# Performance work log

Measured on AMD Instinct MI355X. Metric: run time of the kernel, lower is better.

The kernel has to match this reference:

```python
import jax, jax.numpy as jnp
import numpy as np
import math

DIM = 1536; NH = 12; HD = 128
F, H, W = 6, 30, 30
S = F * H * W
B = 1
K_LEN = 9900  # hardcoded k_lens in the source forward
EPS_NORM = 1e-6


def _rope_tables(max_len=1024, d=HD):
    # Wan rope_params: three tables of widths d-4*(d//6), 2*(d//6), 2*(d//6)
    # -> cos/sin tables of half-widths 22, 21, 21 (concat = d//2 = 64)
    def ang(dd):
        inv = 1.0 / (10000.0 ** (np.arange(0, dd, 2, dtype=np.float64) / dd))
        return np.outer(np.arange(max_len, dtype=np.float64), inv)
    a = np.concatenate([ang(d - 4 * (d // 6)), ang(2 * (d // 6)), ang(2 * (d // 6))], axis=1)
    return np.cos(a).astype(np.float32), np.sin(a).astype(np.float32)


def setup_inputs() -> dict:
    key = jax.random.key(0)
    ks = jax.random.split(key, 5)
    s = 1.0 / math.sqrt(DIM)
    cos, sin = _rope_tables()
    return {
        "x": jax.random.normal(ks[0], (B, S, DIM), jnp.float32),
        "q_w": jax.random.normal(ks[1], (DIM, DIM), jnp.float32) * s,
        "q_b": jnp.zeros((DIM,), jnp.float32),
        "k_w": jax.random.normal(ks[2], (DIM, DIM), jnp.float32) * s,
        "k_b": jnp.zeros((DIM,), jnp.float32),
        "v_w": jax.random.normal(ks[3], (DIM, DIM), jnp.float32) * s,
        "v_b": jnp.zeros((DIM,), jnp.float32),
        "o_w": jax.random.normal(ks[4], (DIM, DIM), jnp.float32) * s,
        "o_b": jnp.zeros((DIM,), jnp.float32),
        "norm_q_w": jnp.ones((DIM,), jnp.float32),
        "norm_k_w": jnp.ones((DIM,), jnp.float32),
        "freqs_cos": jnp.asarray(cos),
        "freqs_sin": jnp.asarray(sin),
        "grid_f": F, "grid_h": H, "grid_w": W,
    }


def rms_norm(x, w):
    # RMSNorm over full model dim, computed in fp32 (as in source)
    xf = x.astype(jnp.float32)
    xn = xf * jax.lax.rsqrt(jnp.mean(xf * xf, axis=-1, keepdims=True) + EPS_NORM)
    return xn.astype(x.dtype) * w


def rope_apply(x, cos, sin, f, h, w):
    # x: [B,S,N,D]; rotate consecutive pairs with 3D-factorized (f,h,w) freqs
    Bb, Ss, Nn, Dd = x.shape
    c = Dd // 2
    sp = [c - 2 * (c // 3), c // 3, c // 3]  # 22, 21, 21

    def grid(tab):
        tf = tab[:, :sp[0]]
        th = tab[:, sp[0]:sp[0] + sp[1]]
        tw = tab[:, sp[0] + sp[1]:]
        g = jnp.concatenate([
            jnp.broadcast_to(tf[:f, None, None, :], (f, h, w, sp[0])),
            jnp.broadcast_to(th[None, :h, None, :], (f, h, w, sp[1])),
            jnp.broadcast_to(tw[None, None, :w, :], (f, h, w, sp[2])),
        ], axis=-1)
        return g.reshape(f * h * w, 1, c)  # [S,1,c] (broadcast over heads)

    gc, gs = grid(cos), grid(sin)
    xp = x.astype(jnp.float32).reshape(Bb, Ss, Nn, c, 2)
    xr, xi = xp[..., 0], xp[..., 1]
    orr = xr * gc - xi * gs
    oii = xr * gs + xi * gc
    return jnp.stack([orr, oii], axis=-1).reshape(Bb, Ss, Nn, Dd).astype(x.dtype)


def attention(q, k, v, k_len):
    # full attention (window_size=(-1,-1)) with keys masked beyond k_len
    scale = 1.0 / math.sqrt(q.shape[-1])
    att = jnp.einsum('bqnd,bknd->bnqk', q, k) * scale
    valid = jnp.arange(k.shape[1]) < k_len
    att = jnp.where(valid[None, None, None, :], att, jnp.finfo(att.dtype).min)
    p = jax.nn.softmax(att, axis=-1)
    return jnp.einsum('bnqk,bknd->bqnd', p, v)


def reference(x, q_w, q_b, k_w, k_b, v_w, v_b, o_w, o_b, norm_q_w, norm_k_w, freqs_cos, freqs_sin, grid_f, grid_h, grid_w):
    Bb, Ss, _ = x.shape
    q = rms_norm(x @ q_w.T + q_b, norm_q_w).reshape(Bb, Ss, NH, HD)
    k = rms_norm(x @ k_w.T + k_b, norm_k_w).reshape(Bb, Ss, NH, HD)
    v = (x @ v_w.T + v_b).reshape(Bb, Ss, NH, HD)
    q = rope_apply(q, freqs_cos, freqs_sin, grid_f, grid_h, grid_w)
    k = rope_apply(k, freqs_cos, freqs_sin, grid_f, grid_h, grid_w)
    o = attention(q, k, v, K_LEN).reshape(Bb, Ss, NH * HD)
    return o @ o_w.T + o_b
```

## Files before the change

kernel.cpp:

```cpp
#include <hip/hip_runtime.h>

#define DIM 1536
#define NH 12
#define HD 128
#define S_LEN 5400
#define SPAD 5504
#define MPAD 5504
#define NQKV 4608
#define EPS_NORM 1e-6f

typedef __bf16 bf16_t;
typedef __bf16 bf16x8 __attribute__((ext_vector_type(8)));
typedef __bf16 bf16x4 __attribute__((ext_vector_type(4)));
typedef __bf16 bf16x2 __attribute__((ext_vector_type(2)));
typedef float  f32x4  __attribute__((ext_vector_type(4)));
typedef float  f32x16 __attribute__((ext_vector_type(16)));
typedef int    i32x2  __attribute__((ext_vector_type(2)));

#define GLOAD_LDS16(gp, lp) __builtin_amdgcn_global_load_lds( \
    (__attribute__((address_space(1))) void*)(void*)(gp),     \
    (__attribute__((address_space(3))) void*)(lp), 16, 0, 0)

__device__ __forceinline__ unsigned int pkbf(float a, float b) {
  union { bf16x2 h; unsigned int u; } c;
  c.h[0] = (__bf16)a; c.h[1] = (__bf16)b;
  return c.u;
}

__device__ __forceinline__ float xhalf_max(float x) {
  i32x2 r = __builtin_amdgcn_permlane32_swap(__float_as_int(x), __float_as_int(x),
                                             false, false);
  return fmaxf(__int_as_float(r.x), __int_as_float(r.y));
}
__device__ __forceinline__ float xhalf_sum(float x) {
  i32x2 r = __builtin_amdgcn_permlane32_swap(__float_as_int(x), __float_as_int(x),
                                             false, false);
  return __int_as_float(r.x) + __int_as_float(r.y);
}


__global__ __launch_bounds__(256) void cvt_x_kernel(const float* __restrict__ x,
                                                    bf16_t* __restrict__ xb) {
  size_t base = ((size_t)blockIdx.x * 256 + threadIdx.x) * 4;
  if (base >= (size_t)MPAD * DIM) return;
  size_t row = base / DIM;
  float4 v = make_float4(0.f, 0.f, 0.f, 0.f);
  if (row < S_LEN) v = *(const float4*)&x[base];
  bf16x4 o; o[0] = (__bf16)v.x; o[1] = (__bf16)v.y; o[2] = (__bf16)v.z; o[3] = (__bf16)v.w;
  *(bf16x4*)&xb[base] = o;
}

__global__ __launch_bounds__(256) void cvt_wqkv_kernel(const float* __restrict__ qw,
                                                       const float* __restrict__ kw,
                                                       const float* __restrict__ vw,
                                                       bf16_t* __restrict__ wb) {
  size_t base = ((size_t)blockIdx.x * 256 + threadIdx.x) * 4;
  if (base >= (size_t)NQKV * DIM) return;
  int row = (int)(base / DIM);
  int col = (int)(base - (size_t)row * DIM);
  const float* src; int rr = row;
  if (rr >= 3072)      { src = vw; rr -= 3072; }
  else if (rr >= 1536) { src = kw; rr -= 1536; }
  else                 { src = qw; }
  float4 v = *(const float4*)&src[(size_t)rr * DIM + col];
  bf16x4 o; o[0] = (__bf16)v.x; o[1] = (__bf16)v.y; o[2] = (__bf16)v.z; o[3] = (__bf16)v.w;
  *(bf16x4*)&wb[base] = o;
}

__global__ __launch_bounds__(256) void cvt_wo_kernel(const float* __restrict__ w,
                                                     bf16_t* __restrict__ wb) {
  size_t base = ((size_t)blockIdx.x * 256 + threadIdx.x) * 4;
  if (base >= (size_t)DIM * DIM) return;
  float4 v = *(const float4*)&w[base];
  bf16x4 o; o[0] = (__bf16)v.x; o[1] = (__bf16)v.y; o[2] = (__bf16)v.z; o[3] = (__bf16)v.w;
  *(bf16x4*)&wb[base] = o;
}


template<bool OUT_BF16>
__global__ __launch_bounds__(256) void gemm_bt_kernel(
    const bf16_t* __restrict__ A, const bf16_t* __restrict__ B, void* __restrict__ C,
    const float* __restrict__ bias0, const float* __restrict__ bias1,
    const float* __restrict__ bias2, int M, int N, int K, int Mvalid) {
  __shared__ bf16_t As[2][128 * 32];
  __shared__ bf16_t Bs[2][128 * 32];
  int tid = threadIdx.x;
  int lane = tid & 63, wave = tid >> 6, quad = lane >> 4, l16 = lane & 15;
  int m0 = blockIdx.y * 128, n0 = blockIdx.x * 128;
  int wm = (wave >> 1) * 64, wn = (wave & 1) * 64;
  const bf16_t* Ab = A + (size_t)m0 * K;
  const bf16_t* Bb = B + (size_t)n0 * K;
  f32x4 acc[4][4] = {};

  int eo0 = tid * 8;
  int row0 = eo0 >> 5, col0 = eo0 & 31;
  int eo1 = (256 + tid) * 8;
  int row1 = eo1 >> 5, col1 = eo1 & 31;

  GLOAD_LDS16(Ab + (size_t)row0 * K + col0, &As[0][eo0]);
  GLOAD_LDS16(Bb + (size_t)row0 * K + col0, &Bs[0][eo0]);
  GLOAD_LDS16(Ab + (size_t)row1 * K + col1, &As[0][eo1]);
  GLOAD_LDS16(Bb + (size_t)row1 * K + col1, &Bs[0][eo1]);
  asm volatile("s_waitcnt vmcnt(0)" ::: "memory");
  __builtin_amdgcn_s_barrier();
  __builtin_amdgcn_sched_barrier(0);

  int KT = K >> 5;
  for (int t = 0; t < KT; t++) {
    int cur = t & 1;
    if (t + 1 < KT) {
      int kn = (t + 1) << 5;
      GLOAD_LDS16(Ab + (size_t)row0 * K + kn + col0, &As[cur ^ 1][eo0]);
      GLOAD_LDS16(Bb + (size_t)row0 * K + kn + col0, &Bs[cur ^ 1][eo0]);
      GLOAD_LDS16(Ab + (size_t)row1 * K + kn + col1, &As[cur ^ 1][eo1]);
      GLOAD_LDS16(Bb + (size_t)row1 * K + kn + col1, &Bs[cur ^ 1][eo1]);
    }
    bf16x8 af[4], bfr[4];
#pragma unroll
    for (int i = 0; i < 4; i++)
      af[i] = *(const bf16x8*)&As[cur][(wm + i * 16 + l16) * 32 + quad * 8];
#pragma unroll
    for (int j = 0; j < 4; j++)
      bfr[j] = *(const bf16x8*)&Bs[cur][(wn + j * 16 + l16) * 32 + quad * 8];
#pragma unroll
    for (int i = 0; i < 4; i++)
#pragma unroll
      for (int j = 0; j < 4; j++)
        acc[i][j] = __builtin_amdgcn_mfma_f32_16x16x32_bf16(af[i], bfr[j], acc[i][j], 0, 0, 0);
    asm volatile("s_waitcnt vmcnt(0) lgkmcnt(0)" ::: "memory");
    __builtin_amdgcn_s_barrier();
    __builtin_amdgcn_sched_barrier(0);
  }
#pragma unroll
  for (int j = 0; j < 4; j++) {
    int n = n0 + wn + j * 16 + l16;
    float bias = (n < 1536) ? bias0[n] : (n < 3072) ? bias1[n - 1536] : bias2[n - 3072];
#pragma unroll
    for (int i = 0; i < 4; i++) {
#pragma unroll
      for (int r = 0; r < 4; r++) {
        int m = m0 + wm + i * 16 + quad * 4 + r;
        float v = acc[i][j][r] + bias;
        if (OUT_BF16) {
          ((bf16_t*)C)[(size_t)m * N + n] = (__bf16)v;
        } else {
          if (m < Mvalid) ((float*)C)[(size_t)m * N + n] = v;
        }
      }
    }
  }
}


__global__ __launch_bounds__(256) void rope_qk_kernel(
    const bf16_t* __restrict__ qkv, const float* __restrict__ nqw,
    const float* __restrict__ nkw, const float* __restrict__ fcos,
    const float* __restrict__ fsin, bf16_t* __restrict__ qout,
    bf16_t* __restrict__ kout) {
  int s = blockIdx.x;
  int tid = threadIdx.x;
  bool valid = s < S_LEN;
  int f = s / 900, hh = (s / 30) % 30, ww = s % 30;
  __shared__ float red[4];
  for (int which = 0; which < 2; which++) {
    const bf16_t* src = qkv + (size_t)s * NQKV + which * DIM;
    const float* nw = which ? nkw : nqw;
    bf16_t* dst = (which ? kout : qout) + (size_t)s * DIM;
    float osc = which ? 1.0f : 0.12751742686f;
    float v[6]; float ss = 0.f;
#pragma unroll
    for (int i = 0; i < 6; i++) {
      v[i] = valid ? (float)src[tid * 6 + i] : 0.f;
      ss += v[i] * v[i];
    }
#pragma unroll
    for (int off = 32; off >= 1; off >>= 1) ss += __shfl_down(ss, off);
    if ((tid & 63) == 0) red[tid >> 6] = ss;
    __syncthreads();
    float tot = red[0] + red[1] + red[2] + red[3];
    float rn = rsqrtf(tot * (1.f / DIM) + EPS_NORM);
    __syncthreads();
#pragma unroll
    for (int i = 0; i < 3; i++) {
      int e0 = tid * 6 + 2 * i;
      int p = e0 >> 1;
      int cc = p & 63;
      int pos = (cc < 22) ? f : (cc < 43) ? hh : ww;
      float c = fcos[pos * 64 + cc], sn = fsin[pos * 64 + cc];
      float xr = v[2 * i] * rn * nw[e0];
      float xi = v[2 * i + 1] * rn * nw[e0 + 1];
      dst[e0]     = (__bf16)((xr * c - xi * sn) * osc);
      dst[e0 + 1] = (__bf16)((xr * sn + xi * c) * osc);
    }
  }
}


__global__ __launch_bounds__(256) void v_transpose_kernel(const bf16_t* __restrict__ qkv,
                                                          bf16_t* __restrict__ vt) {
  __shared__ bf16_t tile[64][136];
  int h = blockIdx.y, s0 = blockIdx.x * 64, tid = threadIdx.x;
#pragma unroll
  for (int it = 0; it < 4; it++) {
    int eo = (it * 256 + tid) * 8;
    int row = eo >> 7, col = eo & 127;
    int s = s0 + row;
    bf16x8 val = {};
    if (s < S_LEN) val = *(const bf16x8*)&qkv[(size_t)s * NQKV + 3072 + h * HD + col];
    *(bf16x8*)&tile[row][col] = val;
  }
  __syncthreads();
  int d = tid & 127, j0 = (tid >> 7) * 32;
  bf16x8 outv[4];
#pragma unroll
  for (int b = 0; b < 4; b++)
#pragma unroll
    for (int j = 0; j < 8; j++) outv[b][j] = tile[j0 + b * 8 + j][d];
  size_t base = ((size_t)h * HD + d) * SPAD + s0 + j0;
#pragma unroll
  for (int b = 0; b < 4; b++) *(bf16x8*)&vt[base + b * 8] = outv[b];
}


__global__ __launch_bounds__(256, 2) void flash_attn_kernel(
    const bf16_t* __restrict__ q, const bf16_t* __restrict__ k,
    const bf16_t* __restrict__ vt, bf16_t* __restrict__ o) {
  __shared__ __align__(16) char lds_raw[65536];
  bf16_t* Ks = (bf16_t*)lds_raw;
  bf16_t* Vs = (bf16_t*)(lds_raw + 32768);
  int nwg = gridDim.x;
  int bid = blockIdx.x;
  int xcd = bid & 7, idx = bid >> 3;
  int q8 = nwg >> 3, rr = nwg & 7;
  int work = (xcd < rr ? xcd * (q8 + 1) : rr * (q8 + 1) + (xcd - rr) * q8) + idx;
  int head = work / 43;
  int s0 = (work - head * 43) * 128;

  int tid = threadIdx.x, w = tid >> 6, lane = tid & 63;
  int l31 = lane & 31, hh = lane >> 5;

  bf16x8 bq[8];
  {
    const bf16_t* qp = &q[(size_t)(s0 + w * 32 + l31) * DIM + head * HD + hh * 8];
#pragma unroll
    for (int kc = 0; kc < 8; kc++) bq[kc] = *(const bf16x8*)(qp + kc * 16);
  }

  float m_i = -1e30f, l_i = 0.f;
  f32x16 oacc[4] = {};

  const int NT = SPAD / 128;

  for (int t = 0; t < NT; t++) {
    int kt = t * 128;

#pragma unroll
    for (int it = 0; it < 8; it++) {
      int slot = it * 256 + tid;
      int row = slot >> 4, pc = slot & 15;
      int c = pc ^ (row & 15);
      GLOAD_LDS16(k + (size_t)(kt + row) * DIM + head * HD + c * 8, &Ks[slot * 8]);
    }
#pragma unroll
    for (int h2 = 0; h2 < 2; h2++)
#pragma unroll
      for (int it = 0; it < 4; it++) {
        int slot = it * 256 + tid;
        int row = slot >> 4, pc = slot & 15;
        int cp = pc ^ (row & 15);
        int d = 2 * row + (cp >> 3);
        GLOAD_LDS16(vt + ((size_t)head * HD + d) * SPAD + kt + h2 * 64 + (cp & 7) * 8,
                    &Vs[h2 * 8192 + slot * 8]);
      }
    asm volatile("s_waitcnt vmcnt(0)" ::: "memory");
    __builtin_amdgcn_s_barrier();
    __builtin_amdgcn_sched_barrier(0);

    f32x16 sacc[4] = {};
    __builtin_amdgcn_s_setprio(1);
#pragma unroll
    for (int ns = 0; ns < 4; ns++) {
      int row = ns * 32 + l31;
#pragma unroll
      for (int kc = 0; kc < 8; kc++) {
        int pc = (kc * 2 + hh) ^ (row & 15);
        bf16x8 ak = *(const bf16x8*)&Ks[row * 128 + pc * 8];
        sacc[ns] = __builtin_amdgcn_mfma_f32_32x32x16_bf16(ak, bq[kc], sacc[ns], 0, 0, 0);
      }
    }
    __builtin_amdgcn_s_setprio(0);

    if (kt + 128 > S_LEN) {
#pragma unroll
      for (int ns = 0; ns < 4; ns++)
#pragma unroll
        for (int r = 0; r < 16; r++) {
          int kvg = kt + ns * 32 + (r & 3) + 8 * (r >> 2) + 4 * hh;
          if (kvg >= S_LEN) sacc[ns][r] = -1e30f;
        }
    }

    float mx;
    {
      float tm[8];
#pragma unroll
      for (int i = 0; i < 8; i++) {
        float a = fmaxf(fmaxf(sacc[0][i], sacc[0][i + 8]),
                        fmaxf(sacc[1][i], sacc[1][i + 8]));
        float b = fmaxf(fmaxf(sacc[2][i], sacc[2][i + 8]),
                        fmaxf(sacc[3][i], sacc[3][i + 8]));
        tm[i] = fmaxf(a, b);
      }
#pragma unroll
      for (int i = 0; i < 4; i++) tm[i] = fmaxf(tm[i], tm[i + 4]);
      mx = fmaxf(fmaxf(tm[0], tm[2]), fmaxf(tm[1], tm[3]));
    }
    mx = xhalf_max(mx);
    if (!__all(mx - m_i <= 11.5f)) {
      float mn = fmaxf(m_i, mx);
      float al = __builtin_amdgcn_exp2f(m_i - mn);
      l_i *= al;
#pragma unroll
      for (int dt = 0; dt < 4; dt++)
#pragma unroll
        for (int r = 0; r < 16; r++) oacc[dt][r] *= al;
      m_i = mn;
    }
#pragma unroll
    for (int ns = 0; ns < 4; ns++)
#pragma unroll
      for (int r = 0; r < 16; r++)
        sacc[ns][r] = __builtin_amdgcn_exp2f(sacc[ns][r] - m_i);
    float rs;
    {
      float ts[8];
#pragma unroll
      for (int i = 0; i < 8; i++)
        ts[i] = ((sacc[0][i] + sacc[0][i + 8]) + (sacc[1][i] + sacc[1][i + 8])) +
                ((sacc[2][i] + sacc[2][i + 8]) + (sacc[3][i] + sacc[3][i + 8]));
#pragma unroll
      for (int i = 0; i < 4; i++) ts[i] += ts[i + 4];
      rs = (ts[0] + ts[2]) + (ts[1] + ts[3]);
    }
    l_i += xhalf_sum(rs);

    __builtin_amdgcn_s_setprio(1);
#pragma unroll
    for (int kvc = 0; kvc < 8; kvc++) {
      int ns = kvc >> 1, rb = (kvc & 1) * 8;
      int w0 = (int)pkbf(sacc[ns][rb + 0], sacc[ns][rb + 1]);
      int w1 = (int)pkbf(sacc[ns][rb + 2], sacc[ns][rb + 3]);
      int w2 = (int)pkbf(sacc[ns][rb + 4], sacc[ns][rb + 5]);
      int w3 = (int)pkbf(sacc[ns][rb + 6], sacc[ns][rb + 7]);
      i32x2 r02 = __builtin_amdgcn_permlane32_swap(w0, w2, false, false);
      i32x2 r13 = __builtin_amdgcn_permlane32_swap(w1, w3, false, false);
      union { unsigned int u[4]; bf16x8 v8; } bpu;
      bpu.u[0] = (unsigned int)r02.x; bpu.u[1] = (unsigned int)r13.x;
      bpu.u[2] = (unsigned int)r02.y; bpu.u[3] = (unsigned int)r13.y;
      bf16x8 bp = bpu.v8;
      int h2 = kvc >> 2, kvl = kvc & 3;
      const bf16_t* Vh = Vs + h2 * 8192;
#pragma unroll
      for (int dt = 0; dt < 4; dt++) {
        int d = dt * 32 + l31;
        int r = d >> 1;
        int cp = ((d & 1) << 3) | (kvl * 2 + hh);
        int pc = cp ^ (r & 15);
        bf16x8 av = *(const bf16x8*)&Vh[r * 128 + pc * 8];
        oacc[dt] = __builtin_amdgcn_mfma_f32_32x32x16_bf16(av, bp, oacc[dt], 0, 0, 0);
      }
    }
    __builtin_amdgcn_s_setprio(0);

    asm volatile("s_waitcnt lgkmcnt(0)" ::: "memory");
    __builtin_amdgcn_s_barrier();
    __builtin_amdgcn_sched_barrier(0);
  }

  bf16_t* scr = Ks + w * (32 * 64);
  float inv = 1.f / l_i;
  int qr = lane >> 1, seg = lane & 1;
  int srow = s0 + w * 32 + qr;
#pragma unroll
  for (int half = 0; half < 2; half++) {
#pragma unroll
    for (int dl = 0; dl < 2; dl++) {
      int dt = half * 2 + dl;
#pragma unroll
      for (int tt = 0; tt < 4; tt++) {
        bf16x4 v;
#pragma unroll
        for (int r4 = 0; r4 < 4; r4++) v[r4] = (__bf16)(oacc[dt][tt * 4 + r4] * inv);
        int c8 = dl * 8 + 2 * tt + hh;
        int pc8 = c8 ^ (l31 & 15);
        *(bf16x4*)&scr[l31 * 64 + pc8 * 4] = v;
      }
    }
#pragma unroll
    for (int i = 0; i < 4; i++) {
      int c8 = seg * 8 + 2 * i;
      bf16x4 lo = *(const bf16x4*)&scr[qr * 64 + ((c8) ^ (qr & 15)) * 4];
      bf16x4 hi = *(const bf16x4*)&scr[qr * 64 + ((c8 + 1) ^ (qr & 15)) * 4];
      bf16x8 val;
#pragma unroll
      for (int j = 0; j < 4; j++) { val[j] = lo[j]; val[j + 4] = hi[j]; }
      if (srow < S_LEN)
        *(bf16x8*)&o[(size_t)srow * DIM + head * HD + half * 64 + seg * 32 + i * 8] = val;
    }
  }
}


extern "C" void kernel_launch(void* const* d_in, const int* in_sizes, int n_in,
                              void* d_out, int out_size, void* d_ws, size_t ws_size,
                              hipStream_t stream) {
  const float* x    = (const float*)d_in[0];
  const float* q_w  = (const float*)d_in[1];
  const float* q_b  = (const float*)d_in[2];
  const float* k_w  = (const float*)d_in[3];
  const float* k_b  = (const float*)d_in[4];
  const float* v_w  = (const float*)d_in[5];
  const float* v_b  = (const float*)d_in[6];
  const float* o_w  = (const float*)d_in[7];
  const float* o_b  = (const float*)d_in[8];
  const float* nqw  = (const float*)d_in[9];
  const float* nkw  = (const float*)d_in[10];
  const float* fcos = (const float*)d_in[11];
  const float* fsin = (const float*)d_in[12];

  char* ws = (char*)d_ws;
  bf16_t* xb   = (bf16_t*)(ws + 0);
  bf16_t* wqkv = (bf16_t*)(ws + 16908288);
  bf16_t* wob  = (bf16_t*)(ws + 31064064);
  bf16_t* qkv  = (bf16_t*)(ws + 35782656);
  bf16_t* qb   = (bf16_t*)(ws + 86507520);
  bf16_t* kb   = (bf16_t*)(ws + 103415808);
  bf16_t* vtb  = (bf16_t*)(ws + 0);
  bf16_t* aob  = (bf16_t*)(ws + 35782656);

  cvt_x_kernel<<<(MPAD * DIM / 4 + 255) / 256, 256, 0, stream>>>(x, xb);
  cvt_wqkv_kernel<<<(NQKV * DIM / 4 + 255) / 256, 256, 0, stream>>>(q_w, k_w, v_w, wqkv);
  cvt_wo_kernel<<<(DIM * DIM / 4 + 255) / 256, 256, 0, stream>>>(o_w, wob);

  gemm_bt_kernel<true><<<dim3(NQKV / 128, MPAD / 128), 256, 0, stream>>>(
      xb, wqkv, qkv, q_b, k_b, v_b, MPAD, NQKV, DIM, MPAD);

  rope_qk_kernel<<<MPAD, 256, 0, stream>>>(qkv, nqw, nkw, fcos, fsin, qb, kb);
  v_transpose_kernel<<<dim3(SPAD / 64, NH), 256, 0, stream>>>(qkv, vtb);

  flash_attn_kernel<<<dim3((MPAD / 128) * NH), 256, 0, stream>>>(qb, kb, vtb, aob);

  gemm_bt_kernel<false><<<dim3(DIM / 128, MPAD / 128), 256, 0, stream>>>(
      aob, wob, d_out, o_b, o_b, o_b, MPAD, DIM, DIM, S_LEN);
}
```

Before: 657.1 us.

## Load K/V tiles directly from global into registers, dropping LDS staging

Replaces cooperative LDS staging of K and V tiles with per-wave direct global loads into registers. It also halves the KV tile to 64 rows per iteration. This removes the workgroup barriers and LDS traffic each iteration. In exchange, every wave refetches the same K/V data, which multiplies global/L2 traffic, and load latency is no longer overlapped through shared staging.

```diff
diff --git a/kernel.cpp b/kernel.cpp
--- a/kernel.cpp
+++ b/kernel.cpp
@@ -225,9 +225,7 @@
 __global__ __launch_bounds__(256, 2) void flash_attn_kernel(
     const bf16_t* __restrict__ q, const bf16_t* __restrict__ k,
     const bf16_t* __restrict__ vt, bf16_t* __restrict__ o) {
-  __shared__ __align__(16) char lds_raw[65536];
-  bf16_t* Ks = (bf16_t*)lds_raw;
-  bf16_t* Vs = (bf16_t*)(lds_raw + 32768);
+  __shared__ __align__(16) bf16_t scr_all[4][32 * 64];
   int nwg = gridDim.x;
   int bid = blockIdx.x;
   int xcd = bid & 7, idx = bid >> 3;
@@ -246,53 +244,43 @@
     for (int kc = 0; kc < 8; kc++) bq[kc] = *(const bf16x8*)(qp + kc * 16);
   }
 
+  const bf16_t* kp = k + (size_t)l31 * DIM + head * HD + hh * 8;
+  const bf16_t* vp = vt + ((size_t)head * HD + l31) * SPAD + hh * 8;
+
   float m_i = -1e30f, l_i = 0.f;
   f32x16 oacc[4] = {};
 
-  const int NT = SPAD / 128;
+  const int NT = 85;
 
   for (int t = 0; t < NT; t++) {
-    int kt = t * 128;
-
-#pragma unroll
-    for (int it = 0; it < 8; it++) {
-      int slot = it * 256 + tid;
-      int row = slot >> 4, pc = slot & 15;
-      int c = pc ^ (row & 15);
-      GLOAD_LDS16(k + (size_t)(kt + row) * DIM + head * HD + c * 8, &Ks[slot * 8]);
-    }
-#pragma unroll
-    for (int h2 = 0; h2 < 2; h2++)
-#pragma unroll
-      for (int it = 0; it < 4; it++) {
-        int slot = it * 256 + tid;
-        int row = slot >> 4, pc = slot & 15;
-        int cp = pc ^ (row & 15);
-        int d = 2 * row + (cp >> 3);
-        GLOAD_LDS16(vt + ((size_t)head * HD + d) * SPAD + kt + h2 * 64 + (cp & 7) * 8,
-                    &Vs[h2 * 8192 + slot * 8]);
-      }
-    asm volatile("s_waitcnt vmcnt(0)" ::: "memory");
-    __builtin_amdgcn_s_barrier();
-    __builtin_amdgcn_sched_barrier(0);
-
-    f32x16 sacc[4] = {};
+    int kt = t * 64;
+
+    bf16x8 ak[16];
+#pragma unroll
+    for (int ns = 0; ns < 2; ns++)
+#pragma unroll
+      for (int kc = 0; kc < 8; kc++)
+        ak[ns * 8 + kc] = *(const bf16x8*)(kp + (size_t)(kt + ns * 32) * DIM + kc * 16);
+
+    f32x16 sacc[2] = {};
     __builtin_amdgcn_s_setprio(1);
 #pragma unroll
-    for (int ns = 0; ns < 4; ns++) {
-      int row = ns * 32 + l31;
-#pragma unroll
-      for (int kc = 0; kc < 8; kc++) {
-        int pc = (kc * 2 + hh) ^ (row & 15);
-        bf16x8 ak = *(const bf16x8*)&Ks[row * 128 + pc * 8];
-        sacc[ns] = __builtin_amdgcn_mfma_f32_32x32x16_bf16(ak, bq[kc], sacc[ns], 0, 0, 0);
-      }
-    }
+    for (int ns = 0; ns < 2; ns++)
+#pragma unroll
+      for (int kc = 0; kc < 8; kc++)
+        sacc[ns] = __builtin_amdgcn_mfma_f32_32x32x16_bf16(ak[ns * 8 + kc], bq[kc], sacc[ns], 0, 0, 0);
     __builtin_amdgcn_s_setprio(0);
 
-    if (kt + 128 > S_LEN) {
-#pragma unroll
-      for (int ns = 0; ns < 4; ns++)
+    bf16x8 av[16];
+#pragma unroll
+    for (int kvc = 0; kvc < 4; kvc++)
+#pragma unroll
+      for (int dt = 0; dt < 4; dt++)
+        av[kvc * 4 + dt] = *(const bf16x8*)(vp + (size_t)(dt * 32) * SPAD + kt + kvc * 16);
+
+    if (kt + 64 > S_LEN) {
+#pragma unroll
+      for (int ns = 0; ns < 2; ns++)
 #pragma unroll
         for (int r = 0; r < 16; r++) {
           int kvg = kt + ns * 32 + (r & 3) + 8 * (r >> 2) + 4 * hh;
@@ -304,13 +292,9 @@
     {
       float tm[8];
 #pragma unroll
-      for (int i = 0; i < 8; i++) {
-        float a = fmaxf(fmaxf(sacc[0][i], sacc[0][i + 8]),
-                        fmaxf(sacc[1][i], sacc[1][i + 8]));
-        float b = fmaxf(fmaxf(sacc[2][i], sacc[2][i + 8]),
-                        fmaxf(sacc[3][i], sacc[3][i + 8]));
-        tm[i] = fmaxf(a, b);
-      }
+      for (int i = 0; i < 8; i++)
+        tm[i] = fmaxf(fmaxf(sacc[0][i], sacc[0][i + 8]),
+                      fmaxf(sacc[1][i], sacc[1][i + 8]));
 #pragma unroll
       for (int i = 0; i < 4; i++) tm[i] = fmaxf(tm[i], tm[i + 4]);
       mx = fmaxf(fmaxf(tm[0], tm[2]), fmaxf(tm[1], tm[3]));
@@ -327,7 +311,7 @@
       m_i = mn;
     }
 #pragma unroll
-    for (int ns = 0; ns < 4; ns++)
+    for (int ns = 0; ns < 2; ns++)
 #pragma unroll
       for (int r = 0; r < 16; r++)
         sacc[ns][r] = __builtin_amdgcn_exp2f(sacc[ns][r] - m_i);
@@ -336,8 +320,7 @@
       float ts[8];
 #pragma unroll
       for (int i = 0; i < 8; i++)
-        ts[i] = ((sacc[0][i] + sacc[0][i + 8]) + (sacc[1][i] + sacc[1][i + 8])) +
-                ((sacc[2][i] + sacc[2][i + 8]) + (sacc[3][i] + sacc[3][i + 8]));
+        ts[i] = (sacc[0][i] + sacc[0][i + 8]) + (sacc[1][i] + sacc[1][i + 8]);
 #pragma unroll
       for (int i = 0; i < 4; i++) ts[i] += ts[i + 4];
       rs = (ts[0] + ts[2]) + (ts[1] + ts[3]);
@@ -346,7 +329,7 @@
 
     __builtin_amdgcn_s_setprio(1);
 #pragma unroll
-    for (int kvc = 0; kvc < 8; kvc++) {
+    for (int kvc = 0; kvc < 4; kvc++) {
       int ns = kvc >> 1, rb = (kvc & 1) * 8;
       int w0 = (int)pkbf(sacc[ns][rb + 0], sacc[ns][rb + 1]);
       int w1 = (int)pkbf(sacc[ns][rb + 2], sacc[ns][rb + 3]);
@@ -358,26 +341,14 @@
       bpu.u[0] = (unsigned int)r02.x; bpu.u[1] = (unsigned int)r13.x;
       bpu.u[2] = (unsigned int)r02.y; bpu.u[3] = (unsigned int)r13.y;
       bf16x8 bp = bpu.v8;
-      int h2 = kvc >> 2, kvl = kvc & 3;
-      const bf16_t* Vh = Vs + h2 * 8192;
-#pragma unroll
-      for (int dt = 0; dt < 4; dt++) {
-        int d = dt * 32 + l31;
-        int r = d >> 1;
-        int cp = ((d & 1) << 3) | (kvl * 2 + hh);
-        int pc = cp ^ (r & 15);
-        bf16x8 av = *(const bf16x8*)&Vh[r * 128 + pc * 8];
-        oacc[dt] = __builtin_amdgcn_mfma_f32_32x32x16_bf16(av, bp, oacc[dt], 0, 0, 0);
-      }
+#pragma unroll
+      for (int dt = 0; dt < 4; dt++)
+        oacc[dt] = __builtin_amdgcn_mfma_f32_32x32x16_bf16(av[kvc * 4 + dt], bp, oacc[dt], 0, 0, 0);
     }
     __builtin_amdgcn_s_setprio(0);
-
-    asm volatile("s_waitcnt lgkmcnt(0)" ::: "memory");
-    __builtin_amdgcn_s_barrier();
-    __builtin_amdgcn_sched_barrier(0);
-  }
-
-  bf16_t* scr = Ks + w * (32 * 64);
+  }
+
+  bf16_t* scr = scr_all[w];
   float inv = 1.f / l_i;
   int qr = lane >> 1, seg = lane & 1;
   int srow = s0 + w * 32 + qr;
```

New measurement: 1.231 ms. +87.3%, slower.

## Restructure flash attention to single-wave workgroups with 32-row Q and KV tiles

Applied to the files above, without the earlier changes.

The attention kernel moves from 256-thread workgroups covering 128 query rows with shared 128-key K/V tiles to 64-thread single-wavefront workgroups, each handling 32 query rows and streaming 32-key tiles. This removes the workgroup barriers and shrinks LDS per block so more blocks can be resident. In exchange, each K/V tile is no longer shared across four waves, so global and L2 traffic for K and V rises about fourfold. Each tile also has less MFMA work to hide the load latency behind.

```diff
diff --git a/kernel.cpp b/kernel.cpp
--- a/kernel.cpp
+++ b/kernel.cpp
@@ -222,95 +222,78 @@
 }
 
 
-__global__ __launch_bounds__(256, 2) void flash_attn_kernel(
+__global__ __launch_bounds__(64, 2) void flash_attn_kernel(
     const bf16_t* __restrict__ q, const bf16_t* __restrict__ k,
     const bf16_t* __restrict__ vt, bf16_t* __restrict__ o) {
-  __shared__ __align__(16) char lds_raw[65536];
-  bf16_t* Ks = (bf16_t*)lds_raw;
-  bf16_t* Vs = (bf16_t*)(lds_raw + 32768);
-  int nwg = gridDim.x;
+  __shared__ __align__(16) bf16_t Ks[32 * 128];
+  __shared__ __align__(16) bf16_t Vs[64 * 64];
   int bid = blockIdx.x;
-  int xcd = bid & 7, idx = bid >> 3;
-  int q8 = nwg >> 3, rr = nwg & 7;
-  int work = (xcd < rr ? xcd * (q8 + 1) : rr * (q8 + 1) + (xcd - rr) * q8) + idx;
-  int head = work / 43;
-  int s0 = (work - head * 43) * 128;
-
-  int tid = threadIdx.x, w = tid >> 6, lane = tid & 63;
+  int work = (bid & 7) * 258 + (bid >> 3);
+  int head = work / 172;
+  int s0 = (work - head * 172) * 32;
+
+  int lane = threadIdx.x;
   int l31 = lane & 31, hh = lane >> 5;
 
   bf16x8 bq[8];
   {
-    const bf16_t* qp = &q[(size_t)(s0 + w * 32 + l31) * DIM + head * HD + hh * 8];
+    const bf16_t* qp = &q[(size_t)(s0 + l31) * DIM + head * HD + hh * 8];
 #pragma unroll
     for (int kc = 0; kc < 8; kc++) bq[kc] = *(const bf16x8*)(qp + kc * 16);
   }
+
+  const bf16_t* kbase = k + (size_t)head * HD;
+  const bf16_t* vbase = vt + (size_t)head * HD * SPAD;
 
   float m_i = -1e30f, l_i = 0.f;
   f32x16 oacc[4] = {};
 
-  const int NT = SPAD / 128;
+  const int NT = 169;
 
   for (int t = 0; t < NT; t++) {
-    int kt = t * 128;
+    int kt = t * 32;
 
 #pragma unroll
     for (int it = 0; it < 8; it++) {
-      int slot = it * 256 + tid;
+      int slot = it * 64 + lane;
       int row = slot >> 4, pc = slot & 15;
       int c = pc ^ (row & 15);
-      GLOAD_LDS16(k + (size_t)(kt + row) * DIM + head * HD + c * 8, &Ks[slot * 8]);
-    }
-#pragma unroll
-    for (int h2 = 0; h2 < 2; h2++)
-#pragma unroll
-      for (int it = 0; it < 4; it++) {
-        int slot = it * 256 + tid;
-        int row = slot >> 4, pc = slot & 15;
-        int cp = pc ^ (row & 15);
-        int d = 2 * row + (cp >> 3);
-        GLOAD_LDS16(vt + ((size_t)head * HD + d) * SPAD + kt + h2 * 64 + (cp & 7) * 8,
-                    &Vs[h2 * 8192 + slot * 8]);
+      GLOAD_LDS16(kbase + (size_t)(kt + row) * DIM + c * 8, &Ks[slot * 8]);
+    }
+#pragma unroll
+    for (int it = 0; it < 8; it++) {
+      int slot = it * 64 + lane;
+      int row = slot >> 3, pc = slot & 7;
+      int cp = pc ^ (row & 7);
+      int d = 2 * row + (cp >> 2);
+      GLOAD_LDS16(vbase + (size_t)d * SPAD + kt + (cp & 3) * 8, &Vs[slot * 8]);
+    }
+    asm volatile("s_waitcnt vmcnt(0)" ::: "memory");
+    __builtin_amdgcn_sched_barrier(0);
+
+    f32x16 sacc = {};
+    __builtin_amdgcn_s_setprio(1);
+#pragma unroll
+    for (int kc = 0; kc < 8; kc++) {
+      int pc = (kc * 2 + hh) ^ (l31 & 15);
+      bf16x8 ak = *(const bf16x8*)&Ks[l31 * 128 + pc * 8];
+      sacc = __builtin_amdgcn_mfma_f32_32x32x16_bf16(ak, bq[kc], sacc, 0, 0, 0);
+    }
+    __builtin_amdgcn_s_setprio(0);
+
+    if (kt + 32 > S_LEN) {
+#pragma unroll
+      for (int r = 0; r < 16; r++) {
+        int kvg = kt + (r & 3) + 8 * (r >> 2) + 4 * hh;
+        if (kvg >= S_LEN) sacc[r] = -1e30f;
       }
-    asm volatile("s_waitcnt vmcnt(0)" ::: "memory");
-    __builtin_amdgcn_s_barrier();
-    __builtin_amdgcn_sched_barrier(0);
-
-    f32x16 sacc[4] = {};
-    __builtin_amdgcn_s_setprio(1);
-#pragma unroll
-    for (int ns = 0; ns < 4; ns++) {
-      int row = ns * 32 + l31;
-#pragma unroll
-      for (int kc = 0; kc < 8; kc++) {
-        int pc = (kc * 2 + hh) ^ (row & 15);
-        bf16x8 ak = *(const bf16x8*)&Ks[row * 128 + pc * 8];
-        sacc[ns] = __builtin_amdgcn_mfma_f32_32x32x16_bf16(ak, bq[kc], sacc[ns], 0, 0, 0);
-      }
-    }
-    __builtin_amdgcn_s_setprio(0);
-
-    if (kt + 128 > S_LEN) {
-#pragma unroll
-      for (int ns = 0; ns < 4; ns++)
-#pragma unroll
-        for (int r = 0; r < 16; r++) {
-          int kvg = kt + ns * 32 + (r & 3) + 8 * (r >> 2) + 4 * hh;
-          if (kvg >= S_LEN) sacc[ns][r] = -1e30f;
-        }
     }
 
     float mx;
     {
       float tm[8];
 #pragma unroll
-      for (int i = 0; i < 8; i++) {
-        float a = fmaxf(fmaxf(sacc[0][i], sacc[0][i + 8]),
-                        fmaxf(sacc[1][i], sacc[1][i + 8]));
-        float b = fmaxf(fmaxf(sacc[2][i], sacc[2][i + 8]),
-                        fmaxf(sacc[3][i], sacc[3][i + 8]));
-        tm[i] = fmaxf(a, b);
-      }
+      for (int i = 0; i < 8; i++) tm[i] = fmaxf(sacc[i], sacc[i + 8]);
 #pragma unroll
       for (int i = 0; i < 4; i++) tm[i] = fmaxf(tm[i], tm[i + 4]);
       mx = fmaxf(fmaxf(tm[0], tm[2]), fmaxf(tm[1], tm[3]));
@@ -327,17 +310,13 @@
       m_i = mn;
     }
 #pragma unroll
-    for (int ns = 0; ns < 4; ns++)
-#pragma unroll
-      for (int r = 0; r < 16; r++)
-        sacc[ns][r] = __builtin_amdgcn_exp2f(sacc[ns][r] - m_i);
+    for (int r = 0; r < 16; r++)
+      sacc[r] = __builtin_amdgcn_exp2f(sacc[r] - m_i);
     float rs;
     {
       float ts[8];
 #pragma unroll
-      for (int i = 0; i < 8; i++)
-        ts[i] = ((sacc[0][i] + sacc[0][i + 8]) + (sacc[1][i] + sacc[1][i + 8])) +
-                ((sacc[2][i] + sacc[2][i + 8]) + (sacc[3][i] + sacc[3][i + 8]));
+      for (int i = 0; i < 8; i++) ts[i] = sacc[i] + sacc[i + 8];
 #pragma unroll
       for (int i = 0; i < 4; i++) ts[i] += ts[i + 4];
       rs = (ts[0] + ts[2]) + (ts[1] + ts[3]);
@@ -346,41 +325,38 @@
 
     __builtin_amdgcn_s_setprio(1);
 #pragma unroll
-    for (int kvc = 0; kvc < 8; kvc++) {
-      int ns = kvc >> 1, rb = (kvc & 1) * 8;
-      int w0 = (int)pkbf(sacc[ns][rb + 0], sacc[ns][rb + 1]);
-      int w1 = (int)pkbf(sacc[ns][rb + 2], sacc[ns][rb + 3]);
-      int w2 = (int)pkbf(sacc[ns][rb + 4], sacc[ns][rb + 5]);
-      int w3 = (int)pkbf(sacc[ns][rb + 6], sacc[ns][rb + 7]);
+    for (int kvc = 0; kvc < 2; kvc++) {
+      int rb = kvc * 8;
+      int w0 = (int)pkbf(sacc[rb + 0], sacc[rb + 1]);
+      int w1 = (int)pkbf(sacc[rb + 2], sacc[rb + 3]);
+      int w2 = (int)pkbf(sacc[rb + 4], sacc[rb + 5]);
+      int w3 = (int)pkbf(sacc[rb + 6], sacc[rb + 7]);
       i32x2 r02 = __builtin_amdgcn_permlane32_swap(w0, w2, false, false);
       i32x2 r13 = __builtin_amdgcn_permlane32_swap(w1, w3, false, false);
       union { unsigned int u[4]; bf16x8 v8; } bpu;
       bpu.u[0] = (unsigned int)r02.x; bpu.u[1] = (unsigned int)r13.x;
       bpu.u[2] = (unsigned int)r02.y; bpu.u[3] = (unsigned int)r13.y;
       bf16x8 bp = bpu.v8;
-      int h2 = kvc >> 2, kvl = kvc & 3;
-      const bf16_t* Vh = Vs + h2 * 8192;
 #pragma unroll
       for (int dt = 0; dt < 4; dt++) {
         int d = dt * 32 + l31;
         int r = d >> 1;
-        int cp = ((d & 1) << 3) | (kvl * 2 + hh);
-        int pc = cp ^ (r & 15);
-        bf16x8 av = *(const bf16x8*)&Vh[r * 128 + pc * 8];
+        int cp = ((d & 1) << 2) | (kvc * 2 + hh);
+        int pc = cp ^ (r & 7);
+        bf16x8 av = *(const bf16x8*)&Vs[r * 64 + pc * 8];
         oacc[dt] = __builtin_amdgcn_mfma_f32_32x32x16_bf16(av, bp, oacc[dt], 0, 0, 0);
       }
     }
     __builtin_amdgcn_s_setprio(0);
 
     asm volatile("s_waitcnt lgkmcnt(0)" ::: "memory");
-    __builtin_amdgcn_s_barrier();
     __builtin_amdgcn_sched_barrier(0);
   }
 
-  bf16_t* scr = Ks + w * (32 * 64);
+  bf16_t* scr = Ks;
   float inv = 1.f / l_i;
   int qr = lane >> 1, seg = lane & 1;
-  int srow = s0 + w * 32 + qr;
+  int srow = s0 + qr;
 #pragma unroll
   for (int half = 0; half < 2; half++) {
 #pragma unroll
@@ -448,7 +424,7 @@
   rope_qk_kernel<<<MPAD, 256, 0, stream>>>(qkv, nqw, nkw, fcos, fsin, qb, kb);
   v_transpose_kernel<<<dim3(SPAD / 64, NH), 256, 0, stream>>>(qkv, vtb);
 
-  flash_attn_kernel<<<dim3((MPAD / 128) * NH), 256, 0, stream>>>(qb, kb, vtb, aob);
+  flash_attn_kernel<<<dim3(2064), 64, 0, stream>>>(qb, kb, vtb, aob);
 
   gemm_bt_kernel<false><<<dim3(DIM / 128, MPAD / 128), 256, 0, stream>>>(
       aob, wob, d_out, o_b, o_b, o_b, MPAD, DIM, DIM, S_LEN);
```

Result: slower. 769.5 us (+17.1%).
